# Kernel tuning notes

Measured on AMD Instinct MI355X. Metric: run time of the kernel, lower is better.

Reference implementation:

```python
import jax, jax.numpy as jnp
import numpy as np

B, N, D, H, HD, C = 2, 2048, 2048, 16, 128, 128  # batch, seq, embed, heads, head_dim, chunk
EPS = 1e-6


def setup_inputs() -> dict:
    key = jax.random.key(0)
    ks = jax.random.split(key, 9)
    s = 0.02
    x = jax.random.normal(ks[0], (B, N, D), jnp.float32)
    # per-head negative log decay (lambda = exp(log_decay) in (0,1))
    log_decay = -jax.random.uniform(ks[1], (H,), jnp.float32, minval=0.01, maxval=1.0)
    Wq = jax.random.normal(ks[2], (D, D), jnp.float32) * s
    Wk = jax.random.normal(ks[3], (D, D), jnp.float32) * s
    Wv = jax.random.normal(ks[4], (D, D), jnp.float32) * s
    Wo = jax.random.normal(ks[5], (D, D), jnp.float32) * s
    Wg1 = jax.random.normal(ks[6], (D, HD), jnp.float32) * s
    Wg2 = jax.random.normal(ks[7], (HD, D), jnp.float32) * s
    norm_w = jnp.ones((D,), jnp.float32)
    return dict(x=x, log_decay=log_decay, Wq=Wq, Wk=Wk, Wv=Wv, Wo=Wo,
                Wg1=Wg1, Wg2=Wg2, norm_w=norm_w)


def _lasd(q, k, v, ld):
    # causal linear attention with per-head scalar log-decay, chunked scan.
    # q,k,v: [B,N,H,HD]; ld: [H] (negative). Recurrence: S_t = exp(ld)*S_{t-1} + k_t v_t^T; o_t = q_t @ S_t
    nc = N // C
    to_chunks = lambda t: t.reshape(B, nc, C, H, HD).transpose(1, 0, 3, 2, 4)  # [nc,B,H,C,HD]
    qc, kc, vc = map(to_chunks, (q, k, v))
    i = jnp.arange(C, dtype=jnp.float32)
    diff = i[:, None] - i[None, :]                     # [C,C]
    Dm = jnp.exp(jnp.where(diff >= 0, ld[:, None, None] * diff, -jnp.inf))  # [H,C,C]
    dq = jnp.exp(ld[:, None] * (i + 1.0))              # [H,C] decay applied to q vs chunk-start state
    dk = jnp.exp(ld[:, None] * (C - 1.0 - i))          # [H,C] decay applied to k for state update
    dS = jnp.exp(ld * C)                               # [H]   chunk-level state decay

    def step(S, qkv):
        qb, kb, vb = qkv                               # [B,H,C,HD]
        attn = jnp.einsum('bhid,bhjd->bhij', qb, kb) * Dm
        o = jnp.einsum('bhij,bhje->bhie', attn, vb)
        o = o + jnp.einsum('bhid,bhde->bhie', qb * dq[None, :, :, None], S)
        S = S * dS[None, :, None, None] + jnp.einsum('bhjd,bhje->bhde', kb * dk[None, :, :, None], vb)
        return S, o

    S0 = jnp.zeros((B, H, HD, HD), jnp.float32)
    _, o = jax.lax.scan(step, S0, (qc, kc, vc))        # [nc,B,H,C,HD]
    return o.transpose(1, 0, 3, 2, 4).reshape(B, N, H, HD)


def reference(x, log_decay, Wq, Wk, Wv, Wo, Wg1, Wg2, norm_w):
    silu = jax.nn.silu
    q = silu(x @ Wq).reshape(B, N, H, HD)
    k = silu(x @ Wk).reshape(B, N, H, HD)
    v = silu(x @ Wv).reshape(B, N, H, HD)
    o = _lasd(q, k, v, log_decay).reshape(B, N, D)
    gate = jax.nn.sigmoid((x @ Wg1) @ Wg2)             # two stacked linears, no nonlinearity between
    o = o * gate
    o = o * jax.lax.rsqrt(jnp.mean(o * o, axis=-1, keepdims=True) + EPS) * norm_w  # rmsnorm
    return o @ Wo
```

## Files before the change

kernel.cpp:

```cpp
#include <hip/hip_runtime.h>
#include <hip/hip_bf16.h>
#include <cstdint>
#include <cstddef>

#define B_   2
#define N_   2048
#define D_   2048
#define H_   16
#define HD_  128
#define C_   128
#define NC_  16
#define M_   4096
#define QKVG_ 8192

typedef __attribute__((ext_vector_type(8))) short bf16x8;
typedef __attribute__((ext_vector_type(4))) float f32x4;
typedef __attribute__((ext_vector_type(16))) float f32x16;

__device__ __forceinline__ uint16_t f2bf(float f){
  __hip_bfloat16 h = __float2bfloat16(f);
  return *reinterpret_cast<uint16_t*>(&h);
}
__device__ __forceinline__ float bf2f(uint16_t u){
  union { uint32_t i; float f; } v; v.i = ((uint32_t)u) << 16; return v.f;
}

__device__ __forceinline__ void async16(const uint16_t* g, uint16_t* l){
  __builtin_amdgcn_global_load_lds(
      (const __attribute__((address_space(1))) void*)g,
      (__attribute__((address_space(3))) void*)l, 16, 0, 0);
}

__device__ __forceinline__ int swz(int row, int c){
  return row*128 + ((((c >> 3) ^ row) & 15) << 3) + (c & 7);
}

__global__ __launch_bounds__(256) void cast_kernel(
    const float* __restrict__ x, uint16_t* __restrict__ y)
{
  int i = (blockIdx.x*256 + threadIdx.x)*4;
  float4 f = *(const float4*)(x + i);
  ushort4 u;
  u.x = f2bf(f.x); u.y = f2bf(f.y); u.z = f2bf(f.z); u.w = f2bf(f.w);
  *(ushort4*)(y + i) = u;
}

__global__ __launch_bounds__(256)
void prep_weights(const float* __restrict__ Wq, const float* __restrict__ Wk,
                  const float* __restrict__ Wv, const float* __restrict__ Wo,
                  const float* __restrict__ Wg2, const float* __restrict__ Wg1,
                  uint16_t* __restrict__ WT, uint16_t* __restrict__ WoT,
                  uint16_t* __restrict__ Wg2T, uint16_t* __restrict__ Wg1b)
{
  const int z = blockIdx.z;
  const int tx = threadIdx.x & 31;
  const int ty = threadIdx.x >> 5;
  __shared__ uint16_t tile[32][33];

  if (z == 5){
    if (blockIdx.x >= 4) return;
    const int r0 = blockIdx.y*32, c0 = blockIdx.x*32;
    #pragma unroll
    for (int rr = 0; rr < 4; ++rr){
      int r = r0 + ty + rr*8;
      Wg1b[(size_t)r*HD_ + c0 + tx] = f2bf(Wg1[(size_t)r*HD_ + c0 + tx]);
    }
    return;
  }

  const float* src; uint16_t* dst; int R, Cc;
  if (z < 3)      { src = (z==0)?Wq:(z==1)?Wk:Wv; dst = WT + (size_t)z*D_*D_; R = D_; Cc = D_; }
  else if (z == 3){ src = Wo;  dst = WoT;  R = D_;  Cc = D_; }
  else            { if (blockIdx.y >= 4) return;
                    src = Wg2; dst = Wg2T; R = HD_; Cc = D_; }

  const int r0 = blockIdx.y*32, c0 = blockIdx.x*32;
  #pragma unroll
  for (int rr = 0; rr < 4; ++rr){
    int r = ty + rr*8;
    tile[r][tx] = f2bf(src[(size_t)(r0 + r)*Cc + c0 + tx]);
  }
  __syncthreads();
  #pragma unroll
  for (int rr = 0; rr < 4; ++rr){
    int r = ty + rr*8;
    dst[(size_t)(c0 + r)*R + r0 + tx] = tile[tx][r];
  }
}

template<int ACT, int OUTBF>
__global__ __launch_bounds__(256)
void gemm_bt2(const uint16_t* __restrict__ A, const uint16_t* __restrict__ Bt,
              void* __restrict__ Cout, int M, int Ncols, int K, int klen)
{
  __shared__ __align__(16) uint16_t As[128*64];
  __shared__ __align__(16) uint16_t Bs[128*64];
  const int t    = threadIdx.x;
  const int lane = t & 63, wave = t >> 6;
  const int wm = wave >> 1, wn = wave & 1;
  const int row0 = wm*64, col0 = wn*64;
  const int lm = lane & 31, lh = lane >> 5;

  const uint16_t* Ap = A  + (size_t)(blockIdx.y*128)*K;
  const uint16_t* Bp = Bt + (size_t)(blockIdx.x*128)*K;
  const int kbeg = blockIdx.z * klen;

  f32x16 acc[2][2];
  #pragma unroll
  for (int i = 0; i < 2; ++i)
    #pragma unroll
    for (int j = 0; j < 2; ++j)
      #pragma unroll
      for (int r = 0; r < 16; ++r) acc[i][j][r] = 0.f;

  const int srow = t >> 3;
  const int gch  = (t & 7) ^ (srow & 7);
  const size_t aoff0 = (size_t)srow*K + gch*8;

  for (int k0 = kbeg; k0 < kbeg + klen; k0 += 64){
    #pragma unroll
    for (int c = 0; c < 4; ++c){
      async16(Ap + (size_t)(c*32)*K + aoff0 + k0, As + c*2048 + t*8);
      async16(Bp + (size_t)(c*32)*K + aoff0 + k0, Bs + c*2048 + t*8);
    }
    __syncthreads();
    #pragma unroll
    for (int kh = 0; kh < 4; ++kh){
      bf16x8 af[2], bfr[2];
      const int ch = kh*2 + lh;
      #pragma unroll
      for (int i = 0; i < 2; ++i){
        int r = row0 + i*32 + lm;
        af[i] = *(const bf16x8*)(As + r*64 + ((ch ^ (r & 7)) << 3));
      }
      #pragma unroll
      for (int j = 0; j < 2; ++j){
        int r = col0 + j*32 + lm;
        bfr[j] = *(const bf16x8*)(Bs + r*64 + ((ch ^ (r & 7)) << 3));
      }
      #pragma unroll
      for (int i = 0; i < 2; ++i)
        #pragma unroll
        for (int j = 0; j < 2; ++j)
          acc[i][j] = __builtin_amdgcn_mfma_f32_32x32x16_bf16(af[i], bfr[j], acc[i][j], 0, 0, 0);
    }
    __syncthreads();
  }

  const int mode = (ACT == 3) ? ((blockIdx.x < 48) ? 1 : 2) : ACT;
  uint16_t* outb = (uint16_t*)Cout;
  float*    outf = (float*)Cout + (OUTBF ? 0 : (size_t)blockIdx.z*M*Ncols);
  #pragma unroll
  for (int i = 0; i < 2; ++i){
    #pragma unroll
    for (int j = 0; j < 2; ++j){
      #pragma unroll
      for (int r = 0; r < 16; ++r){
        int row = blockIdx.y*128 + row0 + i*32 + (r & 3) + 8*(r >> 2) + 4*lh;
        int col = blockIdx.x*128 + col0 + j*32 + lm;
        float v = acc[i][j][r];
        if (mode == 1)      v = v / (1.f + __expf(-v));
        else if (mode == 2) v = 1.f / (1.f + __expf(-v));
        size_t off = (size_t)row*Ncols + col;
        if (OUTBF) outb[off] = f2bf(v);
        else       outf[off] = v;
      }
    }
  }
}

template<int ACT, int OUTBF>
__global__ __launch_bounds__(512, 2)
void gemm256(const uint16_t* __restrict__ A, const uint16_t* __restrict__ Bt,
             void* __restrict__ Cout, int M, int Ncols, int K, int klen)
{
  __shared__ __align__(16) uint16_t As[2*256*64];
  __shared__ __align__(16) uint16_t Bs[2*256*64];
  const int t    = threadIdx.x;
  const int lane = t & 63, wave = t >> 6;
  const int wm = wave >> 2, wn = wave & 3;
  const int lm = lane & 31, lh = lane >> 5;

  int arow[4], brow[2], sl[4];
  #pragma unroll
  for (int m = 0; m < 4; ++m) arow[m] = (wm*128 + m*32 + lm)*64;
  #pragma unroll
  for (int n = 0; n < 2; ++n) brow[n] = (wn*64 + n*32 + lm)*64;
  #pragma unroll
  for (int kk = 0; kk < 4; ++kk) sl[kk] = ((kk*2 + lh) ^ (lm & 7)) << 3;

  const uint16_t* Ap = A  + (size_t)(blockIdx.y*256)*K;
  const uint16_t* Bp = Bt + (size_t)(blockIdx.x*256)*K;
  const int kbeg = blockIdx.z*klen;
  const int NT   = klen >> 6;

  const int r64  = t >> 3;
  const int gch  = (t & 7) ^ (r64 & 7);
  const size_t srcoff = (size_t)r64*K + gch*8;
  const int ldst = t*8;

  f32x16 acc[4][2];
  #pragma unroll
  for (int m = 0; m < 4; ++m)
    #pragma unroll
    for (int n = 0; n < 2; ++n)
      #pragma unroll
      for (int r = 0; r < 16; ++r) acc[m][n][r] = 0.f;

  auto stageA = [&](size_t kofs, int lb){
    #pragma unroll
    for (int s = 0; s < 4; ++s)
      async16(Ap + (size_t)(s*64)*K + srcoff + kofs, As + lb + s*4096 + ldst);
  };
  auto stageB = [&](size_t kofs, int lb){
    #pragma unroll
    for (int s = 0; s < 4; ++s)
      async16(Bp + (size_t)(s*64)*K + srcoff + kofs, Bs + lb + s*4096 + ldst);
  };

  stageA(kbeg, 0);        stageB(kbeg, 0);
  stageA(kbeg + 64, 16384); stageB(kbeg + 64, 16384);
  asm volatile("s_waitcnt vmcnt(8)" ::: "memory");
  __builtin_amdgcn_s_barrier();
  asm volatile("" ::: "memory");

  bf16x8 afA[4], afB[4], bfr[2][4];
  #pragma unroll
  for (int kk = 0; kk < 4; ++kk) afA[kk] = *(const bf16x8*)(As + arow[0] + sl[kk]);

  #define MFMA8(AF, MI) do {                                                   \
    __builtin_amdgcn_s_setprio(1);                                             \
    _Pragma("unroll") for (int n = 0; n < 2; ++n)                              \
      _Pragma("unroll") for (int kk = 0; kk < 4; ++kk)                         \
        acc[MI][n] = __builtin_amdgcn_mfma_f32_32x32x16_bf16(                  \
            AF[kk], bfr[n][kk], acc[MI][n], 0, 0, 0);                          \
    __builtin_amdgcn_s_setprio(0); } while(0)

  for (int tt = 0; tt < NT; ++tt){
    const int cb = (tt & 1)*16384, nb = cb ^ 16384;
    const uint16_t* Ac = As + cb;
    const uint16_t* Bc = Bs + cb;
    const uint16_t* An = As + nb;

    #pragma unroll
    for (int n = 0; n < 2; ++n)
      #pragma unroll
      for (int kk = 0; kk < 4; ++kk)
        bfr[n][kk] = *(const bf16x8*)(Bc + brow[n] + sl[kk]);
    #pragma unroll
    for (int kk = 0; kk < 4; ++kk) afB[kk] = *(const bf16x8*)(Ac + arow[1] + sl[kk]);
    MFMA8(afA, 0);

    #pragma unroll
    for (int kk = 0; kk < 4; ++kk) afA[kk] = *(const bf16x8*)(Ac + arow[2] + sl[kk]);
    MFMA8(afB, 1);

    #pragma unroll
    for (int kk = 0; kk < 4; ++kk) afB[kk] = *(const bf16x8*)(Ac + arow[3] + sl[kk]);
    MFMA8(afA, 2);
    asm volatile("s_waitcnt lgkmcnt(0)" ::: "memory");
    __builtin_amdgcn_s_barrier();
    asm volatile("" ::: "memory");

    if (tt + 2 < NT){
      const size_t kc = (size_t)kbeg + (size_t)(tt + 2)*64;
      stageA(kc, cb); stageB(kc, cb);
      asm volatile("s_waitcnt vmcnt(8)" ::: "memory");
    } else {
      asm volatile("s_waitcnt vmcnt(0)" ::: "memory");
    }
    __builtin_amdgcn_s_barrier();
    asm volatile("" ::: "memory");
    if (tt + 1 < NT){
      #pragma unroll
      for (int kk = 0; kk < 4; ++kk) afA[kk] = *(const bf16x8*)(An + arow[0] + sl[kk]);
    }
    MFMA8(afB, 3);
  }
  #undef MFMA8

  const int mode = (ACT == 3) ? (((blockIdx.x << 8) < Ncols - 2048) ? 1 : 2) : ACT;
  uint16_t* outb = (uint16_t*)Cout;
  float*    outf = (float*)Cout + (OUTBF ? 0 : (size_t)blockIdx.z*M*Ncols);
  #pragma unroll
  for (int m = 0; m < 4; ++m){
    #pragma unroll
    for (int n = 0; n < 2; ++n){
      #pragma unroll
      for (int r = 0; r < 16; ++r){
        int row = blockIdx.y*256 + wm*128 + m*32 + (r & 3) + 8*(r >> 2) + 4*lh;
        int col = blockIdx.x*256 + wn*64  + n*32 + lm;
        float v = acc[m][n][r];
        if (mode == 1)      v = v / (1.f + __expf(-v));
        else if (mode == 2) v = 1.f / (1.f + __expf(-v));
        size_t off = (size_t)row*Ncols + col;
        if (OUTBF) outb[off] = f2bf(v);
        else       outf[off] = v;
      }
    }
  }
}

__global__ __launch_bounds__(256)
void add_kernel(const float* __restrict__ p0, const float* __restrict__ p1,
                float* __restrict__ out)
{
  int i = (blockIdx.x*256 + threadIdx.x)*4;
  float4 a = *(const float4*)(p0 + i);
  float4 b = *(const float4*)(p1 + i);
  float4 o; o.x = a.x+b.x; o.y = a.y+b.y; o.z = a.z+b.z; o.w = a.w+b.w;
  *(float4*)(out + i) = o;
}

__global__ __launch_bounds__(256)
void chunk_state_kernel(const uint16_t* __restrict__ qkvg,
                        const float* __restrict__ log_decay, uint16_t* __restrict__ MsumT)
{
  __shared__ __align__(16) uint16_t vT[128*128];
  __shared__ __align__(16) uint16_t kT[128*128];
  const int h = blockIdx.x, b = blockIdx.y, ic = blockIdx.z;
  const int t    = threadIdx.x;
  const int lane = t & 63, wave = t >> 6;
  const int wm = wave >> 1, wn = wave & 1;
  const int e0 = wm*64, d0 = wn*64;
  const int lr = lane & 15, kq = lane >> 4;
  const float ld = log_decay[h];
  const size_t rowbase = (size_t)b*N_ + (size_t)ic*C_;
  const uint16_t* kb = qkvg + (size_t)D_;
  const uint16_t* vb = qkvg + (size_t)2*D_;

  #pragma unroll 4
  for (int it = 0; it < 64; ++it){
    int idx = t + it*256;
    int j = idx >> 7, e = idx & 127;
    uint16_t vv = vb[(rowbase + j)*QKVG_ + h*HD_ + e];
    float kf = bf2f(kb[(rowbase + j)*QKVG_ + h*HD_ + e]) * __expf(ld * (float)(C_ - 1 - j));
    vT[swz(e, j)] = vv;
    kT[swz(e, j)] = f2bf(kf);
  }
  __syncthreads();

  const f32x4 zero = {0.f, 0.f, 0.f, 0.f};
  f32x4 acc[4][4];
  #pragma unroll
  for (int i = 0; i < 4; ++i)
    #pragma unroll
    for (int j = 0; j < 4; ++j) acc[i][j] = zero;

  #pragma unroll
  for (int kt = 0; kt < 4; ++kt){
    bf16x8 af[4], bfr[4];
    #pragma unroll
    for (int i = 0; i < 4; ++i)
      af[i]  = *(const bf16x8*)(vT + swz(e0 + i*16 + lr, kt*32 + kq*8));
    #pragma unroll
    for (int j = 0; j < 4; ++j)
      bfr[j] = *(const bf16x8*)(kT + swz(d0 + j*16 + lr, kt*32 + kq*8));
    #pragma unroll
    for (int i = 0; i < 4; ++i)
      #pragma unroll
      for (int j = 0; j < 4; ++j)
        acc[i][j] = __builtin_amdgcn_mfma_f32_16x16x32_bf16(af[i], bfr[j], acc[i][j], 0, 0, 0);
  }

  uint16_t* Mout = MsumT + (((size_t)ic*B_ + b)*H_ + h)*(size_t)(HD_*HD_);
  #pragma unroll
  for (int i = 0; i < 4; ++i)
    #pragma unroll
    for (int j = 0; j < 4; ++j)
      #pragma unroll
      for (int r = 0; r < 4; ++r)
        Mout[(size_t)(e0 + i*16 + kq*4 + r)*HD_ + d0 + j*16 + lr] = f2bf(acc[i][j][r]);
}

__global__ __launch_bounds__(256)
void scan_kernel(const uint16_t* __restrict__ MsumT, const float* __restrict__ log_decay,
                 uint16_t* __restrict__ StT)
{
  const int h = blockIdx.x, b = blockIdx.y;
  const float ld = log_decay[h];
  const float dS = __expf(ld * (float)C_);
  const int base_e = blockIdx.z*2048;
  float cur[8];
  #pragma unroll
  for (int r = 0; r < 8; ++r) cur[r] = 0.f;
  for (int i = 0; i < NC_; ++i){
    const size_t base = (((size_t)i*B_ + b)*H_ + h)*(size_t)(HD_*HD_) + base_e;
    #pragma unroll
    for (int r = 0; r < 8; ++r){
      int idx = threadIdx.x + r*256;
      StT[base + idx] = f2bf(cur[r]);
      cur[r] = cur[r]*dS + bf2f(MsumT[base + idx]);
    }
  }
}

__global__ __launch_bounds__(256)
void attn_kernel(const uint16_t* __restrict__ qkvg, const uint16_t* __restrict__ StT,
                 const float* __restrict__ log_decay, float* __restrict__ o_attn)
{
  __shared__ __align__(16) uint16_t Ps[128*128];
  __shared__ __align__(16) uint16_t vT[128*128];
  const int h = blockIdx.x, b = blockIdx.y, ic = blockIdx.z;
  const int t    = threadIdx.x;
  const int lane = t & 63, wave = t >> 6;
  const int wm = wave >> 1, wn = wave & 1;
  const int row0 = wm*64, col0 = wn*64;
  const int lr = lane & 15, kq = lane >> 4;
  const float ld = log_decay[h];
  const size_t rowbase = (size_t)b*N_ + (size_t)ic*C_;
  const uint16_t* qb = qkvg;
  const uint16_t* kb = qkvg + (size_t)D_;
  const uint16_t* vb = qkvg + (size_t)2*D_;

  #pragma unroll 4
  for (int it = 0; it < 64; ++it){
    int idx = t + it*256;
    int j = idx >> 7, e = idx & 127;
    vT[swz(e, j)] = vb[(rowbase + j)*QKVG_ + h*HD_ + e];
  }

  const f32x4 zero = {0.f, 0.f, 0.f, 0.f};
  f32x4 acc[4][4];
  #pragma unroll
  for (int i = 0; i < 4; ++i)
    #pragma unroll
    for (int j = 0; j < 4; ++j) acc[i][j] = zero;

  #pragma unroll
  for (int kt = 0; kt < 4; ++kt){
    bf16x8 af[4], bfr[4];
    #pragma unroll
    for (int i = 0; i < 4; ++i)
      af[i]  = *(const bf16x8*)(qb + (rowbase + row0 + i*16 + lr)*QKVG_ + h*HD_ + kt*32 + kq*8);
    #pragma unroll
    for (int j = 0; j < 4; ++j)
      bfr[j] = *(const bf16x8*)(kb + (rowbase + col0 + j*16 + lr)*QKVG_ + h*HD_ + kt*32 + kq*8);
    #pragma unroll
    for (int i = 0; i < 4; ++i)
      #pragma unroll
      for (int j = 0; j < 4; ++j)
        acc[i][j] = __builtin_amdgcn_mfma_f32_16x16x32_bf16(af[i], bfr[j], acc[i][j], 0, 0, 0);
  }
  #pragma unroll
  for (int i = 0; i < 4; ++i)
    #pragma unroll
    for (int j = 0; j < 4; ++j)
      #pragma unroll
      for (int r = 0; r < 4; ++r){
        int row = row0 + i*16 + kq*4 + r;
        int col = col0 + j*16 + lr;
        int dlt = row - col;
        float f = (dlt >= 0) ? __expf(ld * (float)dlt) : 0.f;
        Ps[swz(row, col)] = f2bf(acc[i][j][r] * f);
      }

  #pragma unroll
  for (int i = 0; i < 4; ++i)
    #pragma unroll
    for (int j = 0; j < 4; ++j) acc[i][j] = zero;
  const uint16_t* Sb = StT + (((size_t)ic*B_ + b)*H_ + h)*(size_t)(HD_*HD_);
  #pragma unroll
  for (int kt = 0; kt < 4; ++kt){
    bf16x8 af[4], bfr[4];
    #pragma unroll
    for (int i = 0; i < 4; ++i)
      af[i]  = *(const bf16x8*)(qb + (rowbase + row0 + i*16 + lr)*QKVG_ + h*HD_ + kt*32 + kq*8);
    #pragma unroll
    for (int j = 0; j < 4; ++j)
      bfr[j] = *(const bf16x8*)(Sb + (size_t)(col0 + j*16 + lr)*HD_ + kt*32 + kq*8);
    #pragma unroll
    for (int i = 0; i < 4; ++i)
      #pragma unroll
      for (int j = 0; j < 4; ++j)
        acc[i][j] = __builtin_amdgcn_mfma_f32_16x16x32_bf16(af[i], bfr[j], acc[i][j], 0, 0, 0);
  }
  #pragma unroll
  for (int i = 0; i < 4; ++i)
    #pragma unroll
    for (int r = 0; r < 4; ++r){
      float dqv = __expf(ld * (float)(row0 + i*16 + kq*4 + r + 1));
      #pragma unroll
      for (int j = 0; j < 4; ++j) acc[i][j][r] *= dqv;
    }

  __syncthreads();

  #pragma unroll
  for (int kt = 0; kt < 4; ++kt){
    bf16x8 af[4], bfr[4];
    #pragma unroll
    for (int i = 0; i < 4; ++i)
      af[i]  = *(const bf16x8*)(Ps + swz(row0 + i*16 + lr, kt*32 + kq*8));
    #pragma unroll
    for (int j = 0; j < 4; ++j)
      bfr[j] = *(const bf16x8*)(vT + swz(col0 + j*16 + lr, kt*32 + kq*8));
    #pragma unroll
    for (int i = 0; i < 4; ++i)
      #pragma unroll
      for (int j = 0; j < 4; ++j)
        acc[i][j] = __builtin_amdgcn_mfma_f32_16x16x32_bf16(af[i], bfr[j], acc[i][j], 0, 0, 0);
  }

  #pragma unroll
  for (int i = 0; i < 4; ++i)
    #pragma unroll
    for (int j = 0; j < 4; ++j)
      #pragma unroll
      for (int r = 0; r < 4; ++r){
        int row = row0 + i*16 + kq*4 + r;
        int col = col0 + j*16 + lr;
        o_attn[(rowbase + row)*D_ + h*HD_ + col] = acc[i][j][r];
      }
}

__global__ __launch_bounds__(256)
void gate_norm_kernel(const float* __restrict__ o_attn, const uint16_t* __restrict__ qkvg,
                      const float* __restrict__ norm_w, uint16_t* __restrict__ on)
{
  const int row = blockIdx.x;
  const int t = threadIdx.x;
  const int c1 = t*4, c2 = 1024 + t*4;
  const float*    orow = o_attn + (size_t)row*D_;
  const uint16_t* grow = qkvg + (size_t)row*QKVG_ + 3*D_;
  float4  o1 = *(const float4*)(orow + c1);
  float4  o2 = *(const float4*)(orow + c2);
  ushort4 g1 = *(const ushort4*)(grow + c1);
  ushort4 g2 = *(const ushort4*)(grow + c2);
  float v[8];
  v[0] = o1.x*bf2f(g1.x); v[1] = o1.y*bf2f(g1.y); v[2] = o1.z*bf2f(g1.z); v[3] = o1.w*bf2f(g1.w);
  v[4] = o2.x*bf2f(g2.x); v[5] = o2.y*bf2f(g2.y); v[6] = o2.z*bf2f(g2.z); v[7] = o2.w*bf2f(g2.w);
  float s = 0.f;
  #pragma unroll
  for (int k = 0; k < 8; ++k) s += v[k]*v[k];
  #pragma unroll
  for (int off = 32; off > 0; off >>= 1) s += __shfl_down(s, off);
  __shared__ float red[4];
  if ((t & 63) == 0) red[t >> 6] = s;
  __syncthreads();
  float total = red[0] + red[1] + red[2] + red[3];
  float scale = rsqrtf(total * (1.f/(float)D_) + 1e-6f);
  float4 w1 = *(const float4*)(norm_w + c1);
  float4 w2 = *(const float4*)(norm_w + c2);
  ushort4 b1, b2;
  b1.x = f2bf(v[0]*scale*w1.x); b1.y = f2bf(v[1]*scale*w1.y);
  b1.z = f2bf(v[2]*scale*w1.z); b1.w = f2bf(v[3]*scale*w1.w);
  b2.x = f2bf(v[4]*scale*w2.x); b2.y = f2bf(v[5]*scale*w2.y);
  b2.z = f2bf(v[6]*scale*w2.z); b2.w = f2bf(v[7]*scale*w2.w);
  *(ushort4*)(on + (size_t)row*D_ + c1) = b1;
  *(ushort4*)(on + (size_t)row*D_ + c2) = b2;
}

extern "C" void kernel_launch(void* const* d_in, const int* in_sizes, int n_in,
                              void* d_out, int out_size, void* d_ws, size_t ws_size,
                              hipStream_t stream) {
  const float* x         = (const float*)d_in[0];
  const float* log_decay = (const float*)d_in[1];
  const float* Wq        = (const float*)d_in[2];
  const float* Wk        = (const float*)d_in[3];
  const float* Wv        = (const float*)d_in[4];
  const float* Wo        = (const float*)d_in[5];
  const float* Wg1       = (const float*)d_in[6];
  const float* Wg2       = (const float*)d_in[7];
  const float* norm_w    = (const float*)d_in[8];
  float* out = (float*)d_out;

  uint8_t* p = (uint8_t*)d_ws;
  uint16_t* xb    = (uint16_t*)p; p += (size_t)M_*D_*2;
  uint16_t* WT    = (uint16_t*)p; p += (size_t)QKVG_*D_*2;
  uint16_t* WoT   = (uint16_t*)p; p += (size_t)D_*D_*2;
  uint16_t* Wg1b  = (uint16_t*)p; p += (size_t)D_*HD_*2;
  uint16_t* Wg2T  = (uint16_t*)p; p += (size_t)D_*HD_*2;
  uint16_t* qkvg  = (uint16_t*)p; p += (size_t)M_*QKVG_*2;
  uint16_t* MsumT = (uint16_t*)p; p += (size_t)NC_*B_*H_*HD_*HD_*2;
  uint16_t* StT   = (uint16_t*)p; p += (size_t)NC_*B_*H_*HD_*HD_*2;
  float*    o_att = (float*)WT;
  uint16_t* on    = xb;
  float*    part  = (float*)qkvg;

  cast_kernel<<<(M_*D_)/1024, 256, 0, stream>>>(x, xb);
  prep_weights<<<dim3(64, 64, 6), 256, 0, stream>>>(Wq, Wk, Wv, Wo, Wg2, Wg1,
                                                    WT, WoT, Wg2T, Wg1b);

  gemm_bt2<0,1><<<dim3(D_/128, D_/128, 1), 256, 0, stream>>>(
      Wg2T, Wg1b, WT + (size_t)3*D_*D_, D_, D_, HD_, HD_);

  gemm256<3,1><<<dim3(QKVG_/256, M_/256, 1), 512, 0, stream>>>(
      xb, WT, qkvg, M_, QKVG_, D_, D_);

  chunk_state_kernel<<<dim3(H_, B_, NC_), 256, 0, stream>>>(qkvg, log_decay, MsumT);
  scan_kernel<<<dim3(H_, B_, 8), 256, 0, stream>>>(MsumT, log_decay, StT);
  attn_kernel<<<dim3(H_, B_, NC_), 256, 0, stream>>>(qkvg, StT, log_decay, o_att);

  gate_norm_kernel<<<M_, 256, 0, stream>>>(o_att, qkvg, norm_w, on);
  gemm256<0,0><<<dim3(D_/256, M_/256, 2), 512, 0, stream>>>(
      on, WoT, part, M_, D_, D_, D_/2);
  add_kernel<<<(M_*D_)/1024, 256, 0, stream>>>(part, part + (size_t)M_*D_, out);
}
```

Measured before the change: 425.0 us.

## Restructure gemm256 into a 4-stage BK=32 ring pipeline with split A/B prefetch

New measurement: 421.8 us. No clear change (-0.7%).

```diff
diff --git a/kernel.cpp b/kernel.cpp
--- a/kernel.cpp
+++ b/kernel.cpp
@@ -174,29 +174,29 @@
 void gemm256(const uint16_t* __restrict__ A, const uint16_t* __restrict__ Bt,
              void* __restrict__ Cout, int M, int Ncols, int K, int klen)
 {
-  __shared__ __align__(16) uint16_t As[2*256*64];
-  __shared__ __align__(16) uint16_t Bs[2*256*64];
+  __shared__ __align__(16) uint16_t As[4*256*32];
+  __shared__ __align__(16) uint16_t Bs[4*256*32];
   const int t    = threadIdx.x;
   const int lane = t & 63, wave = t >> 6;
   const int wm = wave >> 2, wn = wave & 3;
   const int lm = lane & 31, lh = lane >> 5;
-
-  int arow[4], brow[2], sl[4];
-  #pragma unroll
-  for (int m = 0; m < 4; ++m) arow[m] = (wm*128 + m*32 + lm)*64;
-  #pragma unroll
-  for (int n = 0; n < 2; ++n) brow[n] = (wn*64 + n*32 + lm)*64;
-  #pragma unroll
-  for (int kk = 0; kk < 4; ++kk) sl[kk] = ((kk*2 + lh) ^ (lm & 7)) << 3;
+  const int sel = (lm >> 1) & 3;
+
+  int arow[4], brow[2], sl[2];
+  #pragma unroll
+  for (int m = 0; m < 4; ++m) arow[m] = (wm*128 + m*32 + lm)*32;
+  #pragma unroll
+  for (int n = 0; n < 2; ++n) brow[n] = (wn*64 + n*32 + lm)*32;
+  #pragma unroll
+  for (int kk = 0; kk < 2; ++kk) sl[kk] = ((kk*2 + lh) ^ sel) << 3;
 
   const uint16_t* Ap = A  + (size_t)(blockIdx.y*256)*K;
   const uint16_t* Bp = Bt + (size_t)(blockIdx.x*256)*K;
   const int kbeg = blockIdx.z*klen;
-  const int NT   = klen >> 6;
-
-  const int r64  = t >> 3;
-  const int gch  = (t & 7) ^ (r64 & 7);
-  const size_t srcoff = (size_t)r64*K + gch*8;
+  const int NTK  = klen >> 5;
+
+  const int gch  = (t & 3) ^ ((t >> 3) & 3);
+  const size_t srcoff = (size_t)(t >> 2)*K + gch*8;
   const int ldst = t*8;
 
   f32x16 acc[4][2];
@@ -207,77 +207,70 @@
       #pragma unroll
       for (int r = 0; r < 16; ++r) acc[m][n][r] = 0.f;
 
-  auto stageA = [&](size_t kofs, int lb){
-    #pragma unroll
-    for (int s = 0; s < 4; ++s)
-      async16(Ap + (size_t)(s*64)*K + srcoff + kofs, As + lb + s*4096 + ldst);
+  auto stageA = [&](int j){
+    const size_t ko = (size_t)kbeg + (size_t)j*32;
+    uint16_t* d = As + (j & 3)*8192 + ldst;
+    async16(Ap + srcoff + ko, d);
+    async16(Ap + (size_t)128*K + srcoff + ko, d + 4096);
   };
-  auto stageB = [&](size_t kofs, int lb){
-    #pragma unroll
-    for (int s = 0; s < 4; ++s)
-      async16(Bp + (size_t)(s*64)*K + srcoff + kofs, Bs + lb + s*4096 + ldst);
+  auto stageB = [&](int j){
+    const size_t ko = (size_t)kbeg + (size_t)j*32;
+    uint16_t* d = Bs + (j & 3)*8192 + ldst;
+    async16(Bp + srcoff + ko, d);
+    async16(Bp + (size_t)128*K + srcoff + ko, d + 4096);
   };
 
-  stageA(kbeg, 0);        stageB(kbeg, 0);
-  stageA(kbeg + 64, 16384); stageB(kbeg + 64, 16384);
+  stageA(0); stageB(0);
+  stageA(1); stageB(1);
+  stageA(2); stageB(2);
   asm volatile("s_waitcnt vmcnt(8)" ::: "memory");
   __builtin_amdgcn_s_barrier();
   asm volatile("" ::: "memory");
 
-  bf16x8 afA[4], afB[4], bfr[2][4];
-  #pragma unroll
-  for (int kk = 0; kk < 4; ++kk) afA[kk] = *(const bf16x8*)(As + arow[0] + sl[kk]);
-
-  #define MFMA8(AF, MI) do {                                                   \
-    __builtin_amdgcn_s_setprio(1);                                             \
-    _Pragma("unroll") for (int n = 0; n < 2; ++n)                              \
-      _Pragma("unroll") for (int kk = 0; kk < 4; ++kk)                         \
-        acc[MI][n] = __builtin_amdgcn_mfma_f32_32x32x16_bf16(                  \
-            AF[kk], bfr[n][kk], acc[MI][n], 0, 0, 0);                          \
-    __builtin_amdgcn_s_setprio(0); } while(0)
-
-  for (int tt = 0; tt < NT; ++tt){
-    const int cb = (tt & 1)*16384, nb = cb ^ 16384;
-    const uint16_t* Ac = As + cb;
-    const uint16_t* Bc = Bs + cb;
-    const uint16_t* An = As + nb;
-
-    #pragma unroll
-    for (int n = 0; n < 2; ++n)
-      #pragma unroll
-      for (int kk = 0; kk < 4; ++kk)
-        bfr[n][kk] = *(const bf16x8*)(Bc + brow[n] + sl[kk]);
-    #pragma unroll
-    for (int kk = 0; kk < 4; ++kk) afB[kk] = *(const bf16x8*)(Ac + arow[1] + sl[kk]);
-    MFMA8(afA, 0);
-
-    #pragma unroll
-    for (int kk = 0; kk < 4; ++kk) afA[kk] = *(const bf16x8*)(Ac + arow[2] + sl[kk]);
-    MFMA8(afB, 1);
-
-    #pragma unroll
-    for (int kk = 0; kk < 4; ++kk) afB[kk] = *(const bf16x8*)(Ac + arow[3] + sl[kk]);
-    MFMA8(afA, 2);
+  for (int kt = 0; kt < NTK; ++kt){
+    const uint16_t* Ac = As + (kt & 3)*8192;
+    const uint16_t* Bc = Bs + (kt & 3)*8192;
+    bf16x8 af[4], bfr[2];
+
+    #pragma unroll
+    for (int m = 0; m < 4; ++m) af[m]  = *(const bf16x8*)(Ac + arow[m] + sl[0]);
+    #pragma unroll
+    for (int n = 0; n < 2; ++n) bfr[n] = *(const bf16x8*)(Bc + brow[n] + sl[0]);
+    if (kt + 3 < NTK) stageA(kt + 3);
+    __builtin_amdgcn_s_barrier();
     asm volatile("s_waitcnt lgkmcnt(0)" ::: "memory");
+    __builtin_amdgcn_sched_barrier(0);
+    __builtin_amdgcn_s_setprio(1);
+    #pragma unroll
+    for (int m = 0; m < 4; ++m)
+      #pragma unroll
+      for (int n = 0; n < 2; ++n)
+        acc[m][n] = __builtin_amdgcn_mfma_f32_32x32x16_bf16(af[m], bfr[n], acc[m][n], 0, 0, 0);
+    __builtin_amdgcn_s_setprio(0);
     __builtin_amdgcn_s_barrier();
     asm volatile("" ::: "memory");
 
-    if (tt + 2 < NT){
-      const size_t kc = (size_t)kbeg + (size_t)(tt + 2)*64;
-      stageA(kc, cb); stageB(kc, cb);
-      asm volatile("s_waitcnt vmcnt(8)" ::: "memory");
-    } else {
-      asm volatile("s_waitcnt vmcnt(0)" ::: "memory");
-    }
+    #pragma unroll
+    for (int m = 0; m < 4; ++m) af[m]  = *(const bf16x8*)(Ac + arow[m] + sl[1]);
+    #pragma unroll
+    for (int n = 0; n < 2; ++n) bfr[n] = *(const bf16x8*)(Bc + brow[n] + sl[1]);
+    if (kt + 3 < NTK) stageB(kt + 3);
+    __builtin_amdgcn_s_barrier();
+    asm volatile("s_waitcnt lgkmcnt(0)" ::: "memory");
+    __builtin_amdgcn_sched_barrier(0);
+    __builtin_amdgcn_s_setprio(1);
+    #pragma unroll
+    for (int m = 0; m < 4; ++m)
+      #pragma unroll
+      for (int n = 0; n < 2; ++n)
+        acc[m][n] = __builtin_amdgcn_mfma_f32_32x32x16_bf16(af[m], bfr[n], acc[m][n], 0, 0, 0);
+    __builtin_amdgcn_s_setprio(0);
+    if (kt + 3 < NTK)      asm volatile("s_waitcnt vmcnt(8)" ::: "memory");
+    else if (kt + 2 < NTK) asm volatile("s_waitcnt vmcnt(4)" ::: "memory");
+    else                   asm volatile("s_waitcnt vmcnt(0)" ::: "memory");
     __builtin_amdgcn_s_barrier();
     asm volatile("" ::: "memory");
-    if (tt + 1 < NT){
-      #pragma unroll
-      for (int kk = 0; kk < 4; ++kk) afA[kk] = *(const bf16x8*)(An + arow[0] + sl[kk]);
-    }
-    MFMA8(afB, 3);
-  }
-  #undef MFMA8
+  }
 
   const int mode = (ACT == 3) ? (((blockIdx.x << 8) < Ncols - 2048) ? 1 : 2) : ACT;
   uint16_t* outb = (uint16_t*)Cout;
```
